# Performance work log

Measured on AMD Instinct MI355X. Metric: run time of the kernel, lower is better.

The kernel has to match this reference:

```python
import jax, jax.numpy as jnp
import numpy as np

W_LOAD = 0.01  # config.w_load
CAP_FACTOR = 2  # expert capacity = CAP_FACTOR * tokens * top_k / n_experts


def setup_inputs() -> dict:
    key = jax.random.key(0)
    ks = jax.random.split(key, 8)
    B, T, d, E, dff = 4, 4096, 1024, 8, 4096
    N = B * T
    s = 0.02
    return {
        "x": jax.random.normal(ks[0], (B, T, d), jnp.float32),
        "noise": jax.random.normal(ks[1], (N, E), jnp.float32),
        "gate_w": jax.random.normal(ks[2], (d, E), jnp.float32) * s,
        "noise_w": jax.random.normal(ks[3], (d, E), jnp.float32) * s,
        "w1": jax.random.normal(ks[4], (E, d, dff), jnp.float32) * s,
        "b1": jnp.zeros((E, dff), jnp.float32),
        "w2": jax.random.normal(ks[5], (E, dff, d), jnp.float32) * s,
        "b2": jnp.zeros((E, d), jnp.float32),
        "top_k": 2,
    }


def _moe_forward(x, noise, gate_w, noise_w, w1, b1, w2, b2, top_k):
    B, T, d = x.shape
    N = B * T
    E = gate_w.shape[1]
    xs = x.reshape(N, d)

    # noisy gating
    gate_logits = xs @ gate_w                       # [N, E]
    noise_std = jax.nn.softplus(xs @ noise_w)       # [N, E]
    gate_logits = gate_logits + noise * noise_std

    # load loss: kth-largest logit excluding each expert i
    eye = jnp.eye(E, dtype=bool)
    masked = jnp.where(eye[None, :, :], -jnp.inf, gate_logits[:, None, :])  # [N,E,E]
    kth_excl = jax.lax.top_k(masked, top_k)[0][..., -1]                     # [N,E]
    P = jax.scipy.stats.norm.cdf((gate_logits - kth_excl) / noise_std)
    load = P.sum(axis=0)                            # [E]
    cv = jnp.std(load, ddof=1) / jnp.mean(load)     # torch .std() is unbiased
    load_loss = W_LOAD * cv ** 2

    # top-k routing weights (softmax over selected logits, in fp32)
    topk_vals, sel = jax.lax.top_k(gate_logits, top_k)          # [N,K]
    wts = jax.nn.softmax(topk_vals.astype(jnp.float32), axis=-1).astype(x.dtype)

    # dispatch: flatten (token, slot) pairs, compute position within each expert
    ef = sel.reshape(-1)                            # [N*K] expert id per pair
    tf = jnp.repeat(jnp.arange(N), top_k)           # [N*K] token id per pair
    wf = wts.reshape(-1)                            # [N*K] combine weight
    oh = jax.nn.one_hot(ef, E, dtype=jnp.int32)     # [N*K, E]
    pos = ((jnp.cumsum(oh, axis=0) - oh) * oh).sum(-1)  # slot index within expert

    C = (CAP_FACTOR * N * top_k) // E               # expert capacity (no drops in practice)
    buf = jnp.zeros((E, C, d), x.dtype).at[ef, pos].set(xs[tf], mode="drop")

    # grouped FFN per expert
    h = jax.nn.gelu(jnp.einsum("ecd,edh->ech", buf, w1) + b1[:, None, :], approximate=True)
    y = jnp.einsum("ech,ehd->ecd", h, w2) + b2[:, None, :]

    # combine: gather pair outputs, weight, scatter-add back to tokens
    valid = pos < C
    pair_out = y[ef, jnp.minimum(pos, C - 1)]       # [N*K, d]
    contrib = jnp.where(valid[:, None], wf[:, None] * pair_out, 0.0)
    results = jnp.zeros((N, d), x.dtype).at[tf].add(contrib)
    return results.reshape(B, T, d), load_loss


def reference(x, noise, gate_w, noise_w, w1, b1, w2, b2, top_k):
    return _moe_forward(x, noise, gate_w, noise_w, w1, b1, w2, b2, top_k)
```

## Files before the change

kernel.cpp:

```cpp
#include <hip/hip_runtime.h>
#include <stdint.h>

#define N_TOK   16384
#define DMODEL  1024
#define NEXP    8
#define DFF     4096
#define CAP     8192
#define MAXB    136
#define W_LOAD_C 0.01f

typedef __attribute__((ext_vector_type(8))) short short8;
typedef __attribute__((ext_vector_type(4))) float f32x4;

__device__ __forceinline__ uint16_t f2bf(float f) {
    uint32_t u = __float_as_uint(f);
    uint32_t r = u + 0x7fffu + ((u >> 16) & 1u);
    return (uint16_t)(r >> 16);
}
__device__ __forceinline__ float bf2f(uint16_t u) {
    return __uint_as_float((uint32_t)u << 16);
}

__device__ __forceinline__ float gelu_tanh(float v) {
    float u = 0.7978845608028654f * (v + 0.044715f * v * v * v);
    float ex = __expf(2.0f * u);
    float th = 1.0f - 2.0f / (ex + 1.0f);
    return 0.5f * v * (1.0f + th);
}

__device__ __forceinline__ void glds16(const uint16_t* g, uint16_t* l) {
    __builtin_amdgcn_global_load_lds(
        (const __attribute__((address_space(1))) void*)g,
        (__attribute__((address_space(3))) void*)l, 16, 0, 0);
}

__global__ __launch_bounds__(512) void gating_kernel(
    const float* __restrict__ x, const float* __restrict__ noise,
    const float* __restrict__ gate_w, const float* __restrict__ noise_w,
    int* __restrict__ cnt, float* __restrict__ loadAcc,
    int* __restrict__ rowlist, float* __restrict__ slotw,
    int* __restrict__ tpos0, int* __restrict__ tpos1,
    float* __restrict__ tw0, float* __restrict__ tw1,
    uint16_t* __restrict__ xb)
{
    __shared__ float lp[8][8];
    __shared__ int   se1[8], se2[8];
    __shared__ float sw1[8], sw2[8];

    const int lane = threadIdx.x & 63;
    const int wid  = threadIdx.x >> 6;
    const int t = blockIdx.x * 8 + wid;

    const float* xr = x + (size_t)t * DMODEL;
    uint16_t* xbr = xb + (size_t)t * DMODEL;
    float ag[8] = {0,0,0,0,0,0,0,0};
    float an[8] = {0,0,0,0,0,0,0,0};
    for (int j = 0; j < 16; ++j) {
        int idx = j * 64 + lane;
        float xv = xr[idx];
        xbr[idx] = f2bf(xv);
        const float4* gp  = (const float4*)(gate_w  + idx * 8);
        const float4* np_ = (const float4*)(noise_w + idx * 8);
        float4 g0 = gp[0], g1 = gp[1];
        float4 n0 = np_[0], n1 = np_[1];
        ag[0] += xv * g0.x; ag[1] += xv * g0.y; ag[2] += xv * g0.z; ag[3] += xv * g0.w;
        ag[4] += xv * g1.x; ag[5] += xv * g1.y; ag[6] += xv * g1.z; ag[7] += xv * g1.w;
        an[0] += xv * n0.x; an[1] += xv * n0.y; an[2] += xv * n0.z; an[3] += xv * n0.w;
        an[4] += xv * n1.x; an[5] += xv * n1.y; an[6] += xv * n1.z; an[7] += xv * n1.w;
    }
    #pragma unroll
    for (int m = 32; m >= 1; m >>= 1) {
        #pragma unroll
        for (int e = 0; e < 8; ++e) {
            ag[e] += __shfl_xor(ag[e], m, 64);
            an[e] += __shfl_xor(an[e], m, 64);
        }
    }
    float logit[8], sdv[8];
    #pragma unroll
    for (int e = 0; e < 8; ++e) {
        float a = an[e];
        float sp = (a > 20.0f) ? a : log1pf(expf(a));
        sdv[e] = sp;
        logit[e] = ag[e] + noise[(size_t)t * 8 + e] * sp;
    }
    float v1 = -1e30f, v2 = -1e30f, v3 = -1e30f; int i1 = 0, i2 = 0;
    #pragma unroll
    for (int e = 0; e < 8; ++e) {
        float v = logit[e];
        if (v > v1)      { v3 = v2; v2 = v1; i2 = i1; v1 = v; i1 = e; }
        else if (v > v2) { v3 = v2; v2 = v; i2 = e; }
        else if (v > v3) { v3 = v; }
    }
    if (lane < 8) {
        float kth = (lane == i1 || lane == i2) ? v3 : v2;
        float z = (logit[lane] - kth) / sdv[lane];
        lp[wid][lane] = 0.5f * erfcf(-z * 0.70710678118654752440f);
    }
    if (lane == 0) {
        float e2 = expf(v2 - v1);
        float inv = 1.0f / (1.0f + e2);
        se1[wid] = i1; se2[wid] = i2;
        sw1[wid] = inv; sw2[wid] = e2 * inv;
        tw0[t] = inv; tw1[t] = e2 * inv;
    }
    __syncthreads();
    if (threadIdx.x < 8) {
        int e = threadIdx.x;
        float s = 0.f;
        #pragma unroll
        for (int w = 0; w < 8; ++w) s += lp[w][e];
        atomicAdd(&loadAcc[e], s);
        int m = 0;
        #pragma unroll
        for (int w = 0; w < 8; ++w) m += (se1[w] == e) + (se2[w] == e);
        if (m > 0) {
            int b = atomicAdd(&cnt[e], m);
            #pragma unroll
            for (int w = 0; w < 8; ++w) {
                int tok = blockIdx.x * 8 + w;
                if (se1[w] == e) {
                    if (b < CAP) { rowlist[e * CAP + b] = tok; slotw[e * CAP + b] = sw1[w]; }
                    tpos0[tok] = e * 32768 + b;
                    b++;
                }
                if (se2[w] == e) {
                    if (b < CAP) { rowlist[e * CAP + b] = tok; slotw[e * CAP + b] = sw2[w]; }
                    tpos1[tok] = e * 32768 + b;
                    b++;
                }
            }
        }
    }
}

__global__ void scan_kernel(const int* __restrict__ cnt,
                            int* __restrict__ be, int* __restrict__ brow,
                            int* __restrict__ ebase)
{
    if (threadIdx.x == 0 && blockIdx.x == 0) {
        int idx = 0;
        for (int e = 0; e < NEXP; ++e) {
            int ce = cnt[e]; if (ce > CAP) ce = CAP;
            int nb = (ce + 255) >> 8;
            ebase[e] = idx * 256;
            for (int k = 0; k < nb; ++k) { be[idx] = e; brow[idx] = k * 256; idx++; }
        }
        for (; idx < MAXB; ++idx) { be[idx] = -1; brow[idx] = 0; }
    }
}

__global__ __launch_bounds__(256) void transpose_w_kernel(
    const float* __restrict__ src, uint16_t* __restrict__ dst, int R, int Cc)
{
    __shared__ float tile[32][33];
    const float* s = src + (size_t)blockIdx.z * R * Cc;
    uint16_t*    d = dst + (size_t)blockIdx.z * R * Cc;
    int c0 = blockIdx.x * 32, r0 = blockIdx.y * 32;
    int tx = threadIdx.x & 31, ty = threadIdx.x >> 5;
    #pragma unroll
    for (int rr = ty; rr < 32; rr += 8)
        tile[rr][tx] = s[(size_t)(r0 + rr) * Cc + c0 + tx];
    __syncthreads();
    #pragma unroll
    for (int rr = ty; rr < 32; rr += 8)
        d[(size_t)(c0 + rr) * R + r0 + tx] = f2bf(tile[tx][rr]);
}

template<int KTOT, int GATHER, int GELU, int ATOMIC>
__global__ __launch_bounds__(512, 1) void gemm_kernel(
    const uint16_t* __restrict__ Abase,
    const uint16_t* __restrict__ Bfull,
    const int*      __restrict__ rowlist,
    const float*    __restrict__ slotw,
    const int*      __restrict__ cnt,
    const int*      __restrict__ be,
    const int*      __restrict__ brow,
    const float*    __restrict__ biasFull,
    uint16_t*       __restrict__ OutBf,
    float*          __restrict__ OutF,
    int ncols, int bo)
{
    __shared__ uint16_t lsm[65536];
    __shared__ int   lT[256];
    __shared__ float lW[256];

    const int nwg  = gridDim.x * gridDim.y;
    const int flat = blockIdx.y * gridDim.x + blockIdx.x;
    const int xcd = flat & 7, sid = flat >> 3;
    const int q = nwg >> 3, r8 = nwg & 7;
    const int f2 = (xcd < r8 ? xcd * (q + 1) : r8 * (q + 1) + (xcd - r8) * q) + sid;
    const int nx  = f2 % gridDim.x;
    const int rbi = f2 / gridDim.x;

    const int rb = rbi + bo;
    if (rb >= MAXB) return;
    const int e = be[rb];
    if (e < 0) return;
    const int row0 = brow[rb];
    int ce = cnt[e]; if (ce > CAP) ce = CAP;
    const int n0 = nx * 256;

    const int t    = threadIdx.x;
    const int lane = t & 63, wid = t >> 6;
    const int fr = lane & 15, ks = lane >> 4;
    const int wr = wid >> 2, wc = wid & 3;

    if (ATOMIC) {
        if (t < 256) {
            int rr = row0 + t;
            int rc = (rr < ce) ? rr : (ce - 1);
            lT[t] = rowlist[e * CAP + rc];
            lW[t] = (rr < ce) ? slotw[e * CAP + rr] : 0.0f;
        }
        __syncthreads();
    }

    const uint16_t* Bp = Bfull + (size_t)e * ncols * KTOT;
    const int rsub = lane >> 2;
    const int kof  = ((lane & 3) ^ (((lane >> 5) & 1) << 1)) * 8;
    const int rowT0 = wid * 16 + rsub;
    const int rowT1 = 128 + wid * 16 + rsub;
    size_t gr0, gr1;
    if (GATHER) {
        int r0c = row0 + rowT0; r0c = (r0c < ce) ? r0c : (ce - 1);
        int r1c = row0 + rowT1; r1c = (r1c < ce) ? r1c : (ce - 1);
        gr0 = (size_t)rowlist[e * CAP + r0c];
        gr1 = (size_t)rowlist[e * CAP + r1c];
    } else {
        gr0 = (size_t)rbi * 256 + rowT0;
        gr1 = (size_t)rbi * 256 + rowT1;
    }
    const uint16_t* srcA0 = Abase + gr0 * KTOT + kof;
    const uint16_t* srcA1 = Abase + gr1 * KTOT + kof;
    const uint16_t* srcB0 = Bp + (size_t)(n0 + rowT0) * KTOT + kof;
    const uint16_t* srcB1 = Bp + (size_t)(n0 + rowT1) * KTOT + kof;
    const int dA0 = wid * 1024 + lane * 16;
    const int dA1 = (8 + wid) * 1024 + lane * 16;
    const int dB0 = 16384 + dA0;
    const int dB1 = 16384 + dA1;

    const int sw = (ks * 16) ^ ((fr >> 3) << 5);
    int aOff[8], bOff[4];
    #pragma unroll
    for (int m = 0; m < 8; ++m) aOff[m] = (wr * 8 + m) * 1024 + fr * 64 + sw;
    #pragma unroll
    for (int n = 0; n < 4; ++n) bOff[n] = 16384 + (wc * 4 + n) * 1024 + fr * 64 + sw;

    f32x4 acc[8][4];
    #pragma unroll
    for (int a = 0; a < 8; ++a)
        #pragma unroll
        for (int b = 0; b < 4; ++b) acc[a][b] = (f32x4){0.f, 0.f, 0.f, 0.f};

    constexpr int NKT = KTOT / 32;
    char* lsb = (char*)lsm;

    #pragma unroll
    for (int p = 0; p < 3; ++p) {
        char* db = lsb + p * 32768;
        glds16(srcA0 + p * 32, (uint16_t*)(db + dA0));
        glds16(srcA1 + p * 32, (uint16_t*)(db + dA1));
        glds16(srcB0 + p * 32, (uint16_t*)(db + dB0));
        glds16(srcB1 + p * 32, (uint16_t*)(db + dB1));
    }
    asm volatile("s_waitcnt vmcnt(8)" ::: "memory");
    __builtin_amdgcn_s_barrier();
    asm volatile("" ::: "memory");

    for (int kt = 0; kt < NKT; ++kt) {
        const char* sb = lsb + (kt & 3) * 32768;
        char* db = lsb + ((kt + 3) & 3) * 32768;
        const bool st3 = (kt + 3) < NKT;
        const int ko = (kt + 3) * 32;
        short8 bf[4], af[4];

        if (st3) {
            glds16(srcA0 + ko, (uint16_t*)(db + dA0));
            glds16(srcA1 + ko, (uint16_t*)(db + dA1));
        }
        #pragma unroll
        for (int n = 0; n < 4; ++n) bf[n] = *(const short8*)(sb + bOff[n]);
        #pragma unroll
        for (int m = 0; m < 4; ++m) af[m] = *(const short8*)(sb + aOff[m]);
        __builtin_amdgcn_s_setprio(1);
        #pragma unroll
        for (int m = 0; m < 4; ++m)
            #pragma unroll
            for (int n = 0; n < 4; ++n)
                acc[m][n] = __builtin_amdgcn_mfma_f32_16x16x32_bf16(
                    af[m], bf[n], acc[m][n], 0, 0, 0);
        __builtin_amdgcn_s_setprio(0);
        asm volatile("" ::: "memory");
        __builtin_amdgcn_s_barrier();
        asm volatile("" ::: "memory");

        if (st3) {
            glds16(srcB0 + ko, (uint16_t*)(db + dB0));
            glds16(srcB1 + ko, (uint16_t*)(db + dB1));
        }
        #pragma unroll
        for (int m = 0; m < 4; ++m) af[m] = *(const short8*)(sb + aOff[4 + m]);
        __builtin_amdgcn_s_setprio(1);
        #pragma unroll
        for (int m = 0; m < 4; ++m)
            #pragma unroll
            for (int n = 0; n < 4; ++n)
                acc[4 + m][n] = __builtin_amdgcn_mfma_f32_16x16x32_bf16(
                    af[m], bf[n], acc[4 + m][n], 0, 0, 0);
        __builtin_amdgcn_s_setprio(0);
        const int rem = NKT - 1 - kt;
        if (rem >= 3)      asm volatile("s_waitcnt vmcnt(8)" ::: "memory");
        else if (rem == 2) asm volatile("s_waitcnt vmcnt(4)" ::: "memory");
        else if (rem == 1) asm volatile("s_waitcnt vmcnt(0)" ::: "memory");
        asm volatile("" ::: "memory");
        __builtin_amdgcn_s_barrier();
        asm volatile("" ::: "memory");
    }

    const float* bias = biasFull + (size_t)e * ncols;
    if (ATOMIC) {
        #pragma unroll
        for (int mi = 0; mi < 8; ++mi) {
            const int rbase = wr * 128 + mi * 16 + ks * 4;
            #pragma unroll
            for (int ni = 0; ni < 4; ++ni) {
                const int c = n0 + wc * 64 + ni * 16 + fr;
                const float bv = bias[c];
                #pragma unroll
                for (int j = 0; j < 4; ++j) {
                    const int rl = rbase + j;
                    if (row0 + rl < ce) {
                        float v = acc[mi][ni][j] + bv;
                        atomicAdd(&OutF[(size_t)lT[rl] * DMODEL + c], lW[rl] * v);
                    }
                }
            }
        }
    } else {
        for (int half = 0; half < 2; ++half) {
            __syncthreads();
            if (wr == half) {
                #pragma unroll
                for (int mi = 0; mi < 8; ++mi) {
                    #pragma unroll
                    for (int ni = 0; ni < 4; ++ni) {
                        const int cl = wc * 64 + ni * 16 + fr;
                        const float bv = bias[n0 + cl];
                        #pragma unroll
                        for (int j = 0; j < 4; ++j) {
                            float v = acc[mi][ni][j] + bv;
                            if (GELU) v = gelu_tanh(v);
                            const int rl2 = mi * 16 + ks * 4 + j;
                            lsm[rl2 * 264 + cl] = f2bf(v);
                        }
                    }
                }
            }
            __syncthreads();
            #pragma unroll
            for (int p = 0; p < 8; ++p) {
                const int r2 = p * 16 + (t >> 5);
                const int cg = (t & 31) * 8;
                short8 v = *(const short8*)&lsm[r2 * 264 + cg];
                *(short8*)&OutBf[((size_t)rbi * 256 + half * 128 + r2) * ncols + n0 + cg] = v;
            }
        }
    }
}

__global__ __launch_bounds__(256) void combine_kernel(
    const uint16_t* __restrict__ y2,
    const int* __restrict__ tpos0, const int* __restrict__ tpos1,
    const float* __restrict__ tw0, const float* __restrict__ tw1,
    const int* __restrict__ ebase, float* __restrict__ out)
{
    const int wid = threadIdx.x >> 6, lane = threadIdx.x & 63;
    const int t = blockIdx.x * 4 + wid;
    const int p0 = tpos0[t], p1 = tpos1[t];
    const int e0 = p0 >> 15, s0 = p0 & 32767;
    const int e1 = p1 >> 15, s1 = p1 & 32767;
    const bool v0 = s0 < CAP, v1 = s1 < CAP;
    const float w0 = v0 ? tw0[t] : 0.0f;
    const float w1 = v1 ? tw1[t] : 0.0f;
    const uint16_t* r0p = y2 + ((size_t)ebase[e0] + (v0 ? s0 : 0)) * DMODEL;
    const uint16_t* r1p = y2 + ((size_t)ebase[e1] + (v1 ? s1 : 0)) * DMODEL;
    float* op = out + (size_t)t * DMODEL;
    #pragma unroll
    for (int half = 0; half < 2; ++half) {
        const int off = half * 512 + lane * 8;
        short8 a = *(const short8*)(r0p + off);
        short8 b = *(const short8*)(r1p + off);
        float4 o0, o1;
        o0.x = w0 * bf2f((uint16_t)a[0]) + w1 * bf2f((uint16_t)b[0]);
        o0.y = w0 * bf2f((uint16_t)a[1]) + w1 * bf2f((uint16_t)b[1]);
        o0.z = w0 * bf2f((uint16_t)a[2]) + w1 * bf2f((uint16_t)b[2]);
        o0.w = w0 * bf2f((uint16_t)a[3]) + w1 * bf2f((uint16_t)b[3]);
        o1.x = w0 * bf2f((uint16_t)a[4]) + w1 * bf2f((uint16_t)b[4]);
        o1.y = w0 * bf2f((uint16_t)a[5]) + w1 * bf2f((uint16_t)b[5]);
        o1.z = w0 * bf2f((uint16_t)a[6]) + w1 * bf2f((uint16_t)b[6]);
        o1.w = w0 * bf2f((uint16_t)a[7]) + w1 * bf2f((uint16_t)b[7]);
        *(float4*)(op + off)     = o0;
        *(float4*)(op + off + 4) = o1;
    }
}

__global__ void finalize_kernel(const float* __restrict__ loadAcc, float* __restrict__ out) {
    if (threadIdx.x == 0) {
        float m = 0.f;
        #pragma unroll
        for (int e = 0; e < 8; ++e) m += loadAcc[e];
        m *= 0.125f;
        float v = 0.f;
        #pragma unroll
        for (int e = 0; e < 8; ++e) { float d0 = loadAcc[e] - m; v += d0 * d0; }
        v *= (1.0f / 7.0f);
        out[(size_t)N_TOK * DMODEL] = W_LOAD_C * v / (m * m);
    }
}

extern "C" void kernel_launch(void* const* d_in, const int* in_sizes, int n_in,
                              void* d_out, int out_size, void* d_ws, size_t ws_size,
                              hipStream_t stream) {
    const float* x       = (const float*)d_in[0];
    const float* noise   = (const float*)d_in[1];
    const float* gate_w  = (const float*)d_in[2];
    const float* noise_w = (const float*)d_in[3];
    const float* w1      = (const float*)d_in[4];
    const float* b1      = (const float*)d_in[5];
    const float* w2      = (const float*)d_in[6];
    const float* b2      = (const float*)d_in[7];
    float* out = (float*)d_out;
    char* ws = (char*)d_ws;

    int*      cnt     = (int*)(ws + 0);
    float*    loadAcc = (float*)(ws + 256);
    int*      ebase   = (int*)(ws + 512);
    int*      be      = (int*)(ws + 1024);
    int*      brow    = (int*)(ws + 2048);
    int*      rowlist = (int*)(ws + 4096);
    int*      tpos0   = (int*)(ws + 266240);
    int*      tpos1   = (int*)(ws + 331776);
    float*    tw0     = (float*)(ws + 397312);
    float*    tw1     = (float*)(ws + 462848);
    float*    slotw   = (float*)(ws + 528384);
    uint16_t* xb      = (uint16_t*)(ws + 790528);
    uint16_t* w1t     = (uint16_t*)(ws + 34344960);
    uint16_t* w2t     = (uint16_t*)(ws + 101453824);
    uint16_t* h       = (uint16_t*)(ws + 168562688);
    const size_t HOFF = 168562688ull;
    const size_t HSZ  = (size_t)MAXB * 256 * DFF * 2;
    uint16_t* y2      = (uint16_t*)(ws + HOFF + HSZ);
    const size_t Y2SZ = (size_t)MAXB * 256 * DMODEL * 2;
    const bool gatherPath = ws_size >= HOFF + HSZ + Y2SZ;

    hipMemsetAsync(ws, 0, 4096, stream);

    gating_kernel<<<2048, 512, 0, stream>>>(x, noise, gate_w, noise_w,
                                            cnt, loadAcc, rowlist, slotw,
                                            tpos0, tpos1, tw0, tw1, xb);
    scan_kernel<<<1, 64, 0, stream>>>(cnt, be, brow, ebase);
    transpose_w_kernel<<<dim3(128, 32, 8), 256, 0, stream>>>(w1, w1t, 1024, 4096);
    transpose_w_kernel<<<dim3(32, 128, 8), 256, 0, stream>>>(w2, w2t, 4096, 1024);
    finalize_kernel<<<1, 64, 0, stream>>>(loadAcc, out);

    if (gatherPath) {
        gemm_kernel<1024, 1, 1, 0><<<dim3(16, MAXB), 512, 0, stream>>>(
            xb, w1t, rowlist, slotw, cnt, be, brow, b1, h, nullptr, DFF, 0);
        gemm_kernel<4096, 0, 0, 0><<<dim3(4, MAXB), 512, 0, stream>>>(
            h, w2t, rowlist, slotw, cnt, be, brow, b2, y2, nullptr, DMODEL, 0);
        combine_kernel<<<4096, 256, 0, stream>>>(y2, tpos0, tpos1, tw0, tw1,
                                                 ebase, out);
    } else {
        hipMemsetAsync(d_out, 0, (size_t)out_size * sizeof(float), stream);
        size_t avail = (ws_size > HOFF) ? ws_size - HOFF : 0;
        int nch = 8, bpc = (MAXB + 7) / 8;
        for (int c = 1; c <= 8; c <<= 1) {
            int b = (MAXB + c - 1) / c;
            if ((size_t)b * 256 * DFF * 2 <= avail) { nch = c; bpc = b; break; }
        }
        for (int c = 0; c < nch; ++c) {
            int bo = c * bpc;
            if (bo >= MAXB) break;
            gemm_kernel<1024, 1, 1, 0><<<dim3(16, bpc), 512, 0, stream>>>(
                xb, w1t, rowlist, slotw, cnt, be, brow, b1, h, nullptr, DFF, bo);
            gemm_kernel<4096, 0, 0, 1><<<dim3(4, bpc), 512, 0, stream>>>(
                h, w2t, rowlist, slotw, cnt, be, brow, b2, nullptr, out, DMODEL, bo);
        }
    }
}
```

Before: 1.022 ms.

## Prefetch next K-tile A fragments across barrier and restructure GEMM main loop

```diff
diff --git a/kernel.cpp b/kernel.cpp
--- a/kernel.cpp
+++ b/kernel.cpp
@@ -188,8 +188,8 @@
     const int nwg  = gridDim.x * gridDim.y;
     const int flat = blockIdx.y * gridDim.x + blockIdx.x;
     const int xcd = flat & 7, sid = flat >> 3;
-    const int q = nwg >> 3, r8 = nwg & 7;
-    const int f2 = (xcd < r8 ? xcd * (q + 1) : r8 * (q + 1) + (xcd - r8) * q) + sid;
+    const int q = nwg >> 3, r8_ = nwg & 7;
+    const int f2 = (xcd < r8_ ? xcd * (q + 1) : r8_ * (q + 1) + (xcd - r8_) * q) + sid;
     const int nx  = f2 % gridDim.x;
     const int rbi = f2 / gridDim.x;
 
@@ -268,55 +268,76 @@
     __builtin_amdgcn_s_barrier();
     asm volatile("" ::: "memory");
 
-    for (int kt = 0; kt < NKT; ++kt) {
-        const char* sb = lsb + (kt & 3) * 32768;
-        char* db = lsb + ((kt + 3) & 3) * 32768;
-        const bool st3 = (kt + 3) < NKT;
-        const int ko = (kt + 3) * 32;
-        short8 bf[4], af[4];
-
-        if (st3) {
-            glds16(srcA0 + ko, (uint16_t*)(db + dA0));
-            glds16(srcA1 + ko, (uint16_t*)(db + dA1));
-        }
-        #pragma unroll
-        for (int n = 0; n < 4; ++n) bf[n] = *(const short8*)(sb + bOff[n]);
-        #pragma unroll
-        for (int m = 0; m < 4; ++m) af[m] = *(const short8*)(sb + aOff[m]);
-        __builtin_amdgcn_s_setprio(1);
-        #pragma unroll
-        for (int m = 0; m < 4; ++m)
-            #pragma unroll
-            for (int n = 0; n < 4; ++n)
-                acc[m][n] = __builtin_amdgcn_mfma_f32_16x16x32_bf16(
-                    af[m], bf[n], acc[m][n], 0, 0, 0);
-        __builtin_amdgcn_s_setprio(0);
-        asm volatile("" ::: "memory");
-        __builtin_amdgcn_s_barrier();
-        asm volatile("" ::: "memory");
-
-        if (st3) {
-            glds16(srcB0 + ko, (uint16_t*)(db + dB0));
-            glds16(srcB1 + ko, (uint16_t*)(db + dB1));
-        }
-        #pragma unroll
-        for (int m = 0; m < 4; ++m) af[m] = *(const short8*)(sb + aOff[4 + m]);
-        __builtin_amdgcn_s_setprio(1);
-        #pragma unroll
-        for (int m = 0; m < 4; ++m)
-            #pragma unroll
-            for (int n = 0; n < 4; ++n)
-                acc[4 + m][n] = __builtin_amdgcn_mfma_f32_16x16x32_bf16(
-                    af[m], bf[n], acc[4 + m][n], 0, 0, 0);
-        __builtin_amdgcn_s_setprio(0);
-        const int rem = NKT - 1 - kt;
-        if (rem >= 3)      asm volatile("s_waitcnt vmcnt(8)" ::: "memory");
-        else if (rem == 2) asm volatile("s_waitcnt vmcnt(4)" ::: "memory");
-        else if (rem == 1) asm volatile("s_waitcnt vmcnt(0)" ::: "memory");
-        asm volatile("" ::: "memory");
-        __builtin_amdgcn_s_barrier();
-        asm volatile("" ::: "memory");
-    }
+    short8 afloP[4], afloQ[4];
+    #pragma unroll
+    for (int m = 0; m < 4; ++m) afloP[m] = *(const short8*)(lsb + aOff[m]);
+
+#define K_STEP(KT, AFLO_C, AFLO_N)                                          \
+  {                                                                         \
+    const int kt_ = (KT);                                                   \
+    const char* sb = lsb + (kt_ & 3) * 32768;                               \
+    char* db = lsb + ((kt_ + 3) & 3) * 32768;                               \
+    const bool st3 = (kt_ + 3) < NKT;                                       \
+    const int ko = (kt_ + 3) * 32;                                          \
+    short8 bf[4], afhi[4];                                                  \
+        \
+    if (st3) {                                                              \
+      glds16(srcA0 + ko, (uint16_t*)(db + dA0));                            \
+      glds16(srcA1 + ko, (uint16_t*)(db + dA1));                            \
+    }                                                                       \
+    _Pragma("unroll")                                                       \
+    for (int n = 0; n < 4; ++n) bf[n] = *(const short8*)(sb + bOff[n]);     \
+    _Pragma("unroll")                                                       \
+    for (int m = 0; m < 4; ++m) afhi[m] = *(const short8*)(sb + aOff[4+m]); \
+    __builtin_amdgcn_sched_barrier(0);                                      \
+    __builtin_amdgcn_s_setprio(1);                                          \
+    _Pragma("unroll")                                                       \
+    for (int m = 0; m < 4; ++m)                                             \
+      _Pragma("unroll")                                                     \
+      for (int n = 0; n < 4; ++n)                                           \
+        acc[m][n] = __builtin_amdgcn_mfma_f32_16x16x32_bf16(                \
+            AFLO_C[m], bf[n], acc[m][n], 0, 0, 0);                          \
+    __builtin_amdgcn_s_setprio(0);                                          \
+    __builtin_amdgcn_sched_barrier(0);                                      \
+    {                                                                       \
+      const int rem = NKT - 1 - kt_;                                        \
+      if (rem >= 3)      asm volatile("s_waitcnt vmcnt(6)" ::: "memory");   \
+      else if (rem == 2) asm volatile("s_waitcnt vmcnt(4)" ::: "memory");   \
+      else if (rem == 1) asm volatile("s_waitcnt vmcnt(0)" ::: "memory");   \
+    }                                                                       \
+    __builtin_amdgcn_s_barrier();     \
+    asm volatile("" ::: "memory");                                          \
+         \
+    if (st3) {                                                              \
+      glds16(srcB0 + ko, (uint16_t*)(db + dB0));                            \
+      glds16(srcB1 + ko, (uint16_t*)(db + dB1));                            \
+    }                                                                       \
+    if (kt_ + 1 < NKT) {                                                    \
+      const char* sn = lsb + ((kt_ + 1) & 3) * 32768;                       \
+      _Pragma("unroll")                                                     \
+      for (int m = 0; m < 4; ++m)                                           \
+        AFLO_N[m] = *(const short8*)(sn + aOff[m]);                         \
+    }                                                                       \
+    __builtin_amdgcn_sched_barrier(0);                                      \
+    __builtin_amdgcn_s_setprio(1);                                          \
+    _Pragma("unroll")                                                       \
+    for (int m = 0; m < 4; ++m)                                             \
+      _Pragma("unroll")                                                     \
+      for (int n = 0; n < 4; ++n)                                           \
+        acc[4+m][n] = __builtin_amdgcn_mfma_f32_16x16x32_bf16(              \
+            afhi[m], bf[n], acc[4+m][n], 0, 0, 0);                          \
+    __builtin_amdgcn_s_setprio(0);                                          \
+    __builtin_amdgcn_sched_barrier(0);                                      \
+    asm volatile("" ::: "memory");                                          \
+    __builtin_amdgcn_s_barrier();                                           \
+    asm volatile("" ::: "memory");                                          \
+  }
+
+    for (int kt = 0; kt < NKT; kt += 2) {
+        K_STEP(kt,     afloP, afloQ);
+        K_STEP(kt + 1, afloQ, afloP);
+    }
+#undef K_STEP
 
     const float* bias = biasFull + (size_t)e * ncols;
     if (ATOMIC) {
```

Result: no change. 1.010 ms (-1.1%).

## Shrink expert GEMM tiles to 128x128 with two workgroups per CU

Applied to the files above, without the earlier changes.

```diff
diff --git a/kernel.cpp b/kernel.cpp
--- a/kernel.cpp
+++ b/kernel.cpp
@@ -6,7 +6,7 @@
 #define NEXP    8
 #define DFF     4096
 #define CAP     8192
-#define MAXB    136
+#define MAXB2   264
 #define W_LOAD_C 0.01f
 
 typedef __attribute__((ext_vector_type(8))) short short8;
@@ -142,11 +142,11 @@
         int idx = 0;
         for (int e = 0; e < NEXP; ++e) {
             int ce = cnt[e]; if (ce > CAP) ce = CAP;
-            int nb = (ce + 255) >> 8;
-            ebase[e] = idx * 256;
-            for (int k = 0; k < nb; ++k) { be[idx] = e; brow[idx] = k * 256; idx++; }
-        }
-        for (; idx < MAXB; ++idx) { be[idx] = -1; brow[idx] = 0; }
+            int nb = (ce + 127) >> 7;
+            ebase[e] = idx * 128;
+            for (int k = 0; k < nb; ++k) { be[idx] = e; brow[idx] = k * 128; idx++; }
+        }
+        for (; idx < MAXB2; ++idx) { be[idx] = -1; brow[idx] = 0; }
     }
 }
 
@@ -168,7 +168,7 @@
 }
 
 template<int KTOT, int GATHER, int GELU, int ATOMIC>
-__global__ __launch_bounds__(512, 1) void gemm_kernel(
+__global__ __launch_bounds__(256, 2) void gemm_kernel(
     const uint16_t* __restrict__ Abase,
     const uint16_t* __restrict__ Bfull,
     const int*      __restrict__ rowlist,
@@ -181,33 +181,33 @@
     float*          __restrict__ OutF,
     int ncols, int bo)
 {
-    __shared__ uint16_t lsm[65536];
-    __shared__ int   lT[256];
-    __shared__ float lW[256];
+    __shared__ uint16_t lsm[32768];
+    __shared__ int   lT[128];
+    __shared__ float lW[128];
 
     const int nwg  = gridDim.x * gridDim.y;
     const int flat = blockIdx.y * gridDim.x + blockIdx.x;
     const int xcd = flat & 7, sid = flat >> 3;
-    const int q = nwg >> 3, r8 = nwg & 7;
-    const int f2 = (xcd < r8 ? xcd * (q + 1) : r8 * (q + 1) + (xcd - r8) * q) + sid;
+    const int q = nwg >> 3, r8_ = nwg & 7;
+    const int f2 = (xcd < r8_ ? xcd * (q + 1) : r8_ * (q + 1) + (xcd - r8_) * q) + sid;
     const int nx  = f2 % gridDim.x;
     const int rbi = f2 / gridDim.x;
 
     const int rb = rbi + bo;
-    if (rb >= MAXB) return;
+    if (rb >= MAXB2) return;
     const int e = be[rb];
     if (e < 0) return;
     const int row0 = brow[rb];
     int ce = cnt[e]; if (ce > CAP) ce = CAP;
-    const int n0 = nx * 256;
+    const int n0 = nx * 128;
 
     const int t    = threadIdx.x;
     const int lane = t & 63, wid = t >> 6;
     const int fr = lane & 15, ks = lane >> 4;
-    const int wr = wid >> 2, wc = wid & 3;
+    const int wr = wid >> 1, wc = wid & 1;
 
     if (ATOMIC) {
-        if (t < 256) {
+        if (t < 128) {
             int rr = row0 + t;
             int rc = (rr < ce) ? rr : (ce - 1);
             lT[t] = rowlist[e * CAP + rc];
@@ -220,7 +220,7 @@
     const int rsub = lane >> 2;
     const int kof  = ((lane & 3) ^ (((lane >> 5) & 1) << 1)) * 8;
     const int rowT0 = wid * 16 + rsub;
-    const int rowT1 = 128 + wid * 16 + rsub;
+    const int rowT1 = 64 + wid * 16 + rsub;
     size_t gr0, gr1;
     if (GATHER) {
         int r0c = row0 + rowT0; r0c = (r0c < ce) ? r0c : (ce - 1);
@@ -228,28 +228,28 @@
         gr0 = (size_t)rowlist[e * CAP + r0c];
         gr1 = (size_t)rowlist[e * CAP + r1c];
     } else {
-        gr0 = (size_t)rbi * 256 + rowT0;
-        gr1 = (size_t)rbi * 256 + rowT1;
+        gr0 = (size_t)rbi * 128 + rowT0;
+        gr1 = (size_t)rbi * 128 + rowT1;
     }
     const uint16_t* srcA0 = Abase + gr0 * KTOT + kof;
     const uint16_t* srcA1 = Abase + gr1 * KTOT + kof;
     const uint16_t* srcB0 = Bp + (size_t)(n0 + rowT0) * KTOT + kof;
     const uint16_t* srcB1 = Bp + (size_t)(n0 + rowT1) * KTOT + kof;
     const int dA0 = wid * 1024 + lane * 16;
-    const int dA1 = (8 + wid) * 1024 + lane * 16;
-    const int dB0 = 16384 + dA0;
-    const int dB1 = 16384 + dA1;
+    const int dA1 = (4 + wid) * 1024 + lane * 16;
+    const int dB0 = 8192 + dA0;
+    const int dB1 = 8192 + dA1;
 
     const int sw = (ks * 16) ^ ((fr >> 3) << 5);
-    int aOff[8], bOff[4];
-    #pragma unroll
-    for (int m = 0; m < 8; ++m) aOff[m] = (wr * 8 + m) * 1024 + fr * 64 + sw;
-    #pragma unroll
-    for (int n = 0; n < 4; ++n) bOff[n] = 16384 + (wc * 4 + n) * 1024 + fr * 64 + sw;
-
-    f32x4 acc[8][4];
-    #pragma unroll
-    for (int a = 0; a < 8; ++a)
+    int aOff[4], bOff[4];
+    #pragma unroll
+    for (int m = 0; m < 4; ++m) aOff[m] = (wr * 4 + m) * 1024 + fr * 64 + sw;
+    #pragma unroll
+    for (int n = 0; n < 4; ++n) bOff[n] = 8192 + (wc * 4 + n) * 1024 + fr * 64 + sw;
+
+    f32x4 acc[4][4];
+    #pragma unroll
+    for (int a = 0; a < 4; ++a)
         #pragma unroll
         for (int b = 0; b < 4; ++b) acc[a][b] = (f32x4){0.f, 0.f, 0.f, 0.f};
 
@@ -258,7 +258,7 @@
 
     #pragma unroll
     for (int p = 0; p < 3; ++p) {
-        char* db = lsb + p * 32768;
+        char* db = lsb + p * 16384;
         glds16(srcA0 + p * 32, (uint16_t*)(db + dA0));
         glds16(srcA1 + p * 32, (uint16_t*)(db + dA1));
         glds16(srcB0 + p * 32, (uint16_t*)(db + dB0));
@@ -269,20 +269,20 @@
     asm volatile("" ::: "memory");
 
     for (int kt = 0; kt < NKT; ++kt) {
-        const char* sb = lsb + (kt & 3) * 32768;
-        char* db = lsb + ((kt + 3) & 3) * 32768;
-        const bool st3 = (kt + 3) < NKT;
-        const int ko = (kt + 3) * 32;
-        short8 bf[4], af[4];
-
-        if (st3) {
+        const char* sb = lsb + (kt & 3) * 16384;
+        if (kt + 3 < NKT) {
+            char* db = lsb + ((kt + 3) & 3) * 16384;
+            const int ko = (kt + 3) * 32;
             glds16(srcA0 + ko, (uint16_t*)(db + dA0));
             glds16(srcA1 + ko, (uint16_t*)(db + dA1));
-        }
+            glds16(srcB0 + ko, (uint16_t*)(db + dB0));
+            glds16(srcB1 + ko, (uint16_t*)(db + dB1));
+        }
+        short8 af[4], bf[4];
+        #pragma unroll
+        for (int m = 0; m < 4; ++m) af[m] = *(const short8*)(sb + aOff[m]);
         #pragma unroll
         for (int n = 0; n < 4; ++n) bf[n] = *(const short8*)(sb + bOff[n]);
-        #pragma unroll
-        for (int m = 0; m < 4; ++m) af[m] = *(const short8*)(sb + aOff[m]);
         __builtin_amdgcn_s_setprio(1);
         #pragma unroll
         for (int m = 0; m < 4; ++m)
@@ -290,24 +290,6 @@
             for (int n = 0; n < 4; ++n)
                 acc[m][n] = __builtin_amdgcn_mfma_f32_16x16x32_bf16(
                     af[m], bf[n], acc[m][n], 0, 0, 0);
-        __builtin_amdgcn_s_setprio(0);
-        asm volatile("" ::: "memory");
-        __builtin_amdgcn_s_barrier();
-        asm volatile("" ::: "memory");
-
-        if (st3) {
-            glds16(srcB0 + ko, (uint16_t*)(db + dB0));
-            glds16(srcB1 + ko, (uint16_t*)(db + dB1));
-        }
-        #pragma unroll
-        for (int m = 0; m < 4; ++m) af[m] = *(const short8*)(sb + aOff[4 + m]);
-        __builtin_amdgcn_s_setprio(1);
-        #pragma unroll
-        for (int m = 0; m < 4; ++m)
-            #pragma unroll
-            for (int n = 0; n < 4; ++n)
-                acc[4 + m][n] = __builtin_amdgcn_mfma_f32_16x16x32_bf16(
-                    af[m], bf[n], acc[4 + m][n], 0, 0, 0);
         __builtin_amdgcn_s_setprio(0);
         const int rem = NKT - 1 - kt;
         if (rem >= 3)      asm volatile("s_waitcnt vmcnt(8)" ::: "memory");
@@ -321,8 +303,8 @@
     const float* bias = biasFull + (size_t)e * ncols;
     if (ATOMIC) {
         #pragma unroll
-        for (int mi = 0; mi < 8; ++mi) {
-            const int rbase = wr * 128 + mi * 16 + ks * 4;
+        for (int mi = 0; mi < 4; ++mi) {
+            const int rbase = wr * 64 + mi * 16 + ks * 4;
             #pragma unroll
             for (int ni = 0; ni < 4; ++ni) {
                 const int c = n0 + wc * 64 + ni * 16 + fr;
@@ -338,33 +320,29 @@
             }
         }
     } else {
-        for (int half = 0; half < 2; ++half) {
-            __syncthreads();
-            if (wr == half) {
+        __syncthreads();
+        #pragma unroll
+        for (int mi = 0; mi < 4; ++mi) {
+            #pragma unroll
+            for (int ni = 0; ni < 4; ++ni) {
+                const int cl = wc * 64 + ni * 16 + fr;
+                const float bv = bias[n0 + cl];
                 #pragma unroll
-                for (int mi = 0; mi < 8; ++mi) {
-                    #pragma unroll
-                    for (int ni = 0; ni < 4; ++ni) {
-                        const int cl = wc * 64 + ni * 16 + fr;
-                        const float bv = bias[n0 + cl];
-                        #pragma unroll
-                        for (int j = 0; j < 4; ++j) {
-                            float v = acc[mi][ni][j] + bv;
-                            if (GELU) v = gelu_tanh(v);
-                            const int rl2 = mi * 16 + ks * 4 + j;
-                            lsm[rl2 * 264 + cl] = f2bf(v);
-                        }
-                    }
+                for (int j = 0; j < 4; ++j) {
+                    float v = acc[mi][ni][j] + bv;
+                    if (GELU) v = gelu_tanh(v);
+                    const int rl = wr * 64 + mi * 16 + ks * 4 + j;
+                    lsm[rl * 136 + cl] = f2bf(v);
                 }
             }
-            __syncthreads();
-            #pragma unroll
-            for (int p = 0; p < 8; ++p) {
-                const int r2 = p * 16 + (t >> 5);
-                const int cg = (t & 31) * 8;
-                short8 v = *(const short8*)&lsm[r2 * 264 + cg];
-                *(short8*)&OutBf[((size_t)rbi * 256 + half * 128 + r2) * ncols + n0 + cg] = v;
-            }
+        }
+        __syncthreads();
+        const int r2 = t >> 1, hcol = (t & 1) * 64;
+        uint16_t* gp = OutBf + ((size_t)rbi * 128 + r2) * ncols + n0 + hcol;
+        #pragma unroll
+        for (int j2 = 0; j2 < 8; ++j2) {
+            short8 v = *(const short8*)&lsm[r2 * 136 + hcol + j2 * 8];
+            *(short8*)(gp + j2 * 8) = v;
         }
     }
 }
@@ -437,21 +415,21 @@
     float*    loadAcc = (float*)(ws + 256);
     int*      ebase   = (int*)(ws + 512);
     int*      be      = (int*)(ws + 1024);
-    int*      brow    = (int*)(ws + 2048);
-    int*      rowlist = (int*)(ws + 4096);
-    int*      tpos0   = (int*)(ws + 266240);
-    int*      tpos1   = (int*)(ws + 331776);
-    float*    tw0     = (float*)(ws + 397312);
-    float*    tw1     = (float*)(ws + 462848);
-    float*    slotw   = (float*)(ws + 528384);
-    uint16_t* xb      = (uint16_t*)(ws + 790528);
-    uint16_t* w1t     = (uint16_t*)(ws + 34344960);
-    uint16_t* w2t     = (uint16_t*)(ws + 101453824);
-    uint16_t* h       = (uint16_t*)(ws + 168562688);
-    const size_t HOFF = 168562688ull;
-    const size_t HSZ  = (size_t)MAXB * 256 * DFF * 2;
+    int*      brow    = (int*)(ws + 3072);
+    int*      rowlist = (int*)(ws + 8192);
+    int*      tpos0   = (int*)(ws + 270336);
+    int*      tpos1   = (int*)(ws + 335872);
+    float*    tw0     = (float*)(ws + 401408);
+    float*    tw1     = (float*)(ws + 466944);
+    float*    slotw   = (float*)(ws + 532480);
+    uint16_t* xb      = (uint16_t*)(ws + 794624);
+    uint16_t* w1t     = (uint16_t*)(ws + 34349056);
+    uint16_t* w2t     = (uint16_t*)(ws + 101457920);
+    uint16_t* h       = (uint16_t*)(ws + 168566784);
+    const size_t HOFF = 168566784ull;
+    const size_t HSZ  = (size_t)MAXB2 * 128 * DFF * 2;
     uint16_t* y2      = (uint16_t*)(ws + HOFF + HSZ);
-    const size_t Y2SZ = (size_t)MAXB * 256 * DMODEL * 2;
+    const size_t Y2SZ = (size_t)MAXB2 * 128 * DMODEL * 2;
     const bool gatherPath = ws_size >= HOFF + HSZ + Y2SZ;
 
     hipMemsetAsync(ws, 0, 4096, stream);
@@ -465,26 +443,26 @@
     finalize_kernel<<<1, 64, 0, stream>>>(loadAcc, out);
 
     if (gatherPath) {
-        gemm_kernel<1024, 1, 1, 0><<<dim3(16, MAXB), 512, 0, stream>>>(
+        gemm_kernel<1024, 1, 1, 0><<<dim3(32, MAXB2), 256, 0, stream>>>(
             xb, w1t, rowlist, slotw, cnt, be, brow, b1, h, nullptr, DFF, 0);
-        gemm_kernel<4096, 0, 0, 0><<<dim3(4, MAXB), 512, 0, stream>>>(
+        gemm_kernel<4096, 0, 0, 0><<<dim3(8, MAXB2), 256, 0, stream>>>(
             h, w2t, rowlist, slotw, cnt, be, brow, b2, y2, nullptr, DMODEL, 0);
         combine_kernel<<<4096, 256, 0, stream>>>(y2, tpos0, tpos1, tw0, tw1,
                                                  ebase, out);
     } else {
         hipMemsetAsync(d_out, 0, (size_t)out_size * sizeof(float), stream);
         size_t avail = (ws_size > HOFF) ? ws_size - HOFF : 0;
-        int nch = 8, bpc = (MAXB + 7) / 8;
+        int nch = 8, bpc = (MAXB2 + 7) / 8;
         for (int c = 1; c <= 8; c <<= 1) {
-            int b = (MAXB + c - 1) / c;
-            if ((size_t)b * 256 * DFF * 2 <= avail) { nch = c; bpc = b; break; }
+            int b = (MAXB2 + c - 1) / c;
+            if ((size_t)b * 128 * DFF * 2 <= avail) { nch = c; bpc = b; break; }
         }
         for (int c = 0; c < nch; ++c) {
             int bo = c * bpc;
-            if (bo >= MAXB) break;
-            gemm_kernel<1024, 1, 1, 0><<<dim3(16, bpc), 512, 0, stream>>>(
+            if (bo >= MAXB2) break;
+            gemm_kernel<1024, 1, 1, 0><<<dim3(32, bpc), 256, 0, stream>>>(
                 xb, w1t, rowlist, slotw, cnt, be, brow, b1, h, nullptr, DFF, bo);
-            gemm_kernel<4096, 0, 0, 1><<<dim3(4, bpc), 512, 0, stream>>>(
+            gemm_kernel<4096, 0, 0, 1><<<dim3(8, bpc), 256, 0, stream>>>(
                 h, w2t, rowlist, slotw, cnt, be, brow, b2, nullptr, out, DMODEL, bo);
         }
     }
```

Result: slower. 1.086 ms (+6.3%).
